# Optimization experiments

Hardware: AMD Instinct MI355X
Metric: run time of the kernel (lower is better)

Reference implementation:

```python
import jax, jax.numpy as jnp
import numpy as np

# ---- static architecture constants (match init_kwargs) ----
B = 64          # batch
N = 64          # n_particles
D = 3           # n_dimensions
H = 256         # hidden_nf
TE = 128        # t_embed_dims
L = 3           # n_layers
SIGMA = 0.5     # data_sigma
MAX_POS = 10000.0
COORDS_RANGE = 15.0  # standard EGNN coords_range; per-layer = COORDS_RANGE/L


def _fc_edges():
    # fully-connected edges (no self loops) within each sample, flattened node ids
    a = np.arange(N)
    r = np.repeat(a, N); c = np.tile(a, N)
    m = r != c
    r0, c0 = r[m], c[m]                      # [N*(N-1)]
    off = (np.arange(B) * N)[:, None]
    rows = (off + r0[None, :]).reshape(-1)   # [B*N*(N-1)]
    cols = (off + c0[None, :]).reshape(-1)
    return jnp.asarray(rows, jnp.int32), jnp.asarray(cols, jnp.int32)


def setup_inputs() -> dict:
    key = jax.random.key(0)
    ks = jax.random.split(key, 20)
    g = lambda k, shape, fan: jax.random.normal(k, shape, jnp.float32) / np.sqrt(fan)
    rows, cols = _fc_edges()
    return {
        'logt': jax.random.normal(ks[0], (B,), jnp.float32),
        'xs':   jax.random.normal(ks[1], (B, N * D), jnp.float32),
        'Wemb': g(ks[2], (TE, H), TE), 'bemb': jnp.zeros((H,), jnp.float32),
        'We1': g(ks[3], (L, 2 * H + 1, H), 2 * H + 1), 'be1': jnp.zeros((L, H), jnp.float32),
        'We2': g(ks[4], (L, H, H), H),                 'be2': jnp.zeros((L, H), jnp.float32),
        'Wa':  g(ks[5], (L, H, 1), H),                 'ba':  jnp.zeros((L, 1), jnp.float32),
        'Wn1': g(ks[6], (L, 2 * H, H), 2 * H),         'bn1': jnp.zeros((L, H), jnp.float32),
        'Wn2': g(ks[7], (L, H, H), H),                 'bn2': jnp.zeros((L, H), jnp.float32),
        'Wc1': g(ks[8], (L, H, H), H),                 'bc1': jnp.zeros((L, H), jnp.float32),
        'Wc2': g(ks[9], (L, H, 1), H) * 1e-3,          # small-init final coord layer
        'rows': rows, 'cols': cols,
    }


def _egnn_net(t_emb, x_flat, Wemb, bemb, We1, be1, We2, be2, Wa, ba,
              Wn1, bn1, Wn2, bn2, Wc1, bc1, Wc2, rows, cols):
    # x_flat: [B*N, D]; t_emb: [B, TE] -> node features [B*N, H]
    num_nodes = B * N
    h = jnp.repeat(t_emb, N, axis=0) @ Wemb + bemb
    x = x_flat
    cr = COORDS_RANGE / L
    for l in range(L):
        diff = x[rows] - x[cols]                              # [E, D]
        radial = jnp.sum(diff * diff, axis=1, keepdims=True)  # [E, 1]
        diff_n = diff / (jnp.sqrt(radial + 1e-8) + 1.0)       # normalized (norm_constant=1)
        eh = jnp.concatenate([h[rows], h[cols], radial], axis=1)
        m = jax.nn.silu(eh @ We1[l] + be1[l])
        m = jax.nn.silu(m @ We2[l] + be2[l])
        m = m * jax.nn.sigmoid(m @ Wa[l] + ba[l])             # attention gate
        # equivariant coordinate update (tanh-bounded)
        s = jax.nn.silu(m @ Wc1[l] + bc1[l])
        trans = diff_n * jnp.tanh(s @ Wc2[l]) * cr            # [E, D]
        x = x + jax.ops.segment_sum(trans, rows, num_segments=num_nodes)
        # node update with residual
        agg = jax.ops.segment_sum(m, rows, num_segments=num_nodes)
        dh = jax.nn.silu(jnp.concatenate([h, agg], axis=1) @ Wn1[l] + bn1[l]) @ Wn2[l] + bn2[l]
        h = h + dh
    vel = (x - x_flat).reshape(B, N, D)
    vel = vel - jnp.mean(vel, axis=1, keepdims=True)          # remove center of gravity
    return vel.reshape(B, N * D)


def reference(logt, xs, Wemb, bemb, We1, be1, We2, be2, Wa, ba,
              Wn1, bn1, Wn2, bn2, Wc1, bc1, Wc2, rows, cols):
    # sinusoidal time embedding of logt/4
    K = TE // 2
    freqs = (1.0 / MAX_POS) ** (jnp.arange(K, dtype=jnp.float32) / K)
    ang = (logt / 4.0)[:, None] * freqs[None, :]
    t_emb = jnp.concatenate([jnp.cos(ang), jnp.sin(ang)], axis=1)  # [B, TE]
    # EDM preconditioning
    t = jnp.exp(logt)[:, None]                                     # [B, 1]
    c_in = 1.0 / jnp.sqrt(SIGMA ** 2 + t ** 2)
    x_flat = (xs * c_in).reshape(B * N, D)
    net_out = _egnn_net(t_emb, x_flat, Wemb, bemb, We1, be1, We2, be2, Wa, ba,
                        Wn1, bn1, Wn2, bn2, Wc1, bc1, Wc2, rows, cols)
    denom = SIGMA ** 2 + t ** 2
    return xs * (SIGMA ** 2) / denom + net_out * (SIGMA * t) / jnp.sqrt(denom)
```

## Files before the change

### kernel.cpp

```cpp
#include <hip/hip_runtime.h>

typedef unsigned short ushort_t;
typedef __attribute__((ext_vector_type(8))) short s8v;
typedef __attribute__((ext_vector_type(4))) float f4v;
typedef __attribute__((ext_vector_type(2))) unsigned int u32x2;
typedef __attribute__((ext_vector_type(4))) unsigned int u32x4;

#define NNODE 4096
#define HID 256
#define CR_L 5.0f
#define ASTR 528
#define ASTR16 (16 * ASTR)
#define NSTR 1056
#define NSTR16 (16 * NSTR)

__device__ __forceinline__ unsigned int cvt2(float lo, float hi) {
  unsigned int r;
  asm("v_cvt_pk_bf16_f32 %0, %1, %2" : "=v"(r) : "v"(lo), "v"(hi));
  return r;
}
__device__ __forceinline__ ushort_t cvt1(float v) {
  unsigned int r;
  asm("v_cvt_pk_bf16_f32 %0, %1, %2" : "=v"(r) : "v"(v), "v"(v));
  return (ushort_t)r;
}
__device__ __forceinline__ float fast_rcp(float x) {
  float r;
  asm("v_rcp_f32 %0, %1" : "=v"(r) : "v"(x));
  return r;
}
__device__ __forceinline__ float silu_f(float v) { return v * fast_rcp(1.0f + __expf(-v)); }
__device__ __forceinline__ float sigm_f(float v) { return fast_rcp(1.0f + __expf(-v)); }

__device__ __forceinline__ void loadB(s8v bd[4], const char* base, int q) {
#pragma unroll
  for (int nt = 0; nt < 4; ++nt)
    bd[nt] = *(const s8v*)(base + nt * 8192 + q * 1024);
}
__device__ __forceinline__ void mfma_step(const char* Ath, int q, const s8v bc[4], f4v acc[4][4]) {
  s8v a[4];
#pragma unroll
  for (int mt = 0; mt < 4; ++mt)
    a[mt] = *(const s8v*)(Ath + mt * ASTR16 + q * 64);
#pragma unroll
  for (int mt = 0; mt < 4; ++mt)
#pragma unroll
    for (int nt = 0; nt < 4; ++nt)
      acc[mt][nt] = __builtin_amdgcn_mfma_f32_16x16x32_bf16(a[mt], bc[nt], acc[mt][nt], 0, 0, 0);
}

__device__ __forceinline__ void gemm64(const char* Ath, const ushort_t* Bth, f4v acc[4][4]) {
#pragma unroll
  for (int ks = 0; ks < 8; ++ks) {
    s8v a[4], bb[4];
#pragma unroll
    for (int mt = 0; mt < 4; ++mt)
      a[mt] = *(const s8v*)(Ath + mt * ASTR16 + ks * 64);
#pragma unroll
    for (int nt = 0; nt < 4; ++nt)
      bb[nt] = *(const s8v*)(Bth + nt * 4096 + ks * 32);
#pragma unroll
    for (int mt = 0; mt < 4; ++mt)
#pragma unroll
      for (int nt = 0; nt < 4; ++nt)
        acc[mt][nt] = __builtin_amdgcn_mfma_f32_16x16x32_bf16(a[mt], bb[nt], acc[mt][nt], 0, 0, 0);
  }
}

__global__ __launch_bounds__(256) void wconv_kernel(
    const float* __restrict__ We1, const float* __restrict__ We2,
    const float* __restrict__ Wc1, const float* __restrict__ Wn1,
    const float* __restrict__ Wn2, ushort_t* __restrict__ wt) {
  int gid = blockIdx.x * 256 + threadIdx.x;
  int l = gid / 458752;
  int r = gid - l * 458752;
  float v;
  if (r < 131072) {
    int part = r >> 16; int rr = r & 65535; int nn = rr >> 8, k = rr & 255;
    v = We1[(l * 513 + part * 256 + k) * 256 + nn];
  } else if (r < 262144) {
    const float* W = (r < 196608) ? We2 : Wc1;
    int rr = (r < 196608) ? (r - 131072) : (r - 196608);
    int ki = rr & 7, ln = (rr >> 3) & 63, f = rr >> 9;
    int ks = f & 7, n16 = f >> 3;
    int al = ln & 15, ag = ln >> 4;
    int nn = n16 * 16 + al, k = ks * 32 + ag * 8 + ki;
    v = W[(l * 256 + k) * 256 + nn];
  } else if (r < 393216) {
    int rr = r - 262144; int nn = rr >> 9, k = rr & 511;
    v = Wn1[(l * 512 + k) * 256 + nn];
  } else {
    int rr = r - 393216; int nn = rr >> 8, k = rr & 255;
    v = Wn2[(l * 256 + k) * 256 + nn];
  }
  wt[gid] = cvt1(v);
}

__global__ __launch_bounds__(256) void embed_kernel(
    const float* __restrict__ logt, const float* __restrict__ xs,
    const float* __restrict__ Wemb, const float* __restrict__ bemb,
    float* __restrict__ h, float* __restrict__ x0) {
  __shared__ float te[128];
  const int b = blockIdx.x, tid = threadIdx.x;
  const float lt = logt[b];
  if (tid < 64) {
    float fr = powf(1e-4f, (float)tid * (1.0f / 64.0f));
    float ang = lt * 0.25f * fr;
    te[tid] = cosf(ang);
    te[tid + 64] = sinf(ang);
  }
  float tt = expf(lt);
  float cin = 1.0f / sqrtf(0.25f + tt * tt);
  if (tid < 192) x0[b * 192 + tid] = xs[b * 192 + tid] * cin;
  __syncthreads();
  float acc = bemb[tid];
  for (int k = 0; k < 128; ++k) acc += te[k] * Wemb[k * 256 + tid];
  float* hp = h + (b * 64) * 256 + tid;
#pragma unroll 4
  for (int nn = 0; nn < 64; ++nn) hp[nn * 256] = acc;
}

__global__ __launch_bounds__(256) void proj_kernel(
    const float* __restrict__ h, const ushort_t* __restrict__ Bt0,
    const ushort_t* __restrict__ Bt1, const float* __restrict__ be1,
    float* __restrict__ p_r, float* __restrict__ p_c) {
  __shared__ u32x4 AbV[64 * ASTR / 16];
  char* Ab = (char*)AbV;
  const int t = threadIdx.x, lane = t & 63, w = t >> 6;
  const int al = lane & 15, ag = lane >> 4;
  const int mat = blockIdx.x & 1;
  const int R0 = (blockIdx.x >> 1) * 64;
  {
    const int j = t & 63, cc = t >> 6;
    const float4* hv = (const float4*)(h + (R0 + j) * 256) + cc * 16;
    u32x4* wb = (u32x4*)(Ab + j * ASTR + cc * 128);
#pragma unroll
    for (int g = 0; g < 8; ++g) {
      float4 v0 = hv[g * 2], v1 = hv[g * 2 + 1];
      u32x4 q;
      q[0] = cvt2(v0.x, v0.y); q[1] = cvt2(v0.z, v0.w);
      q[2] = cvt2(v1.x, v1.y); q[3] = cvt2(v1.z, v1.w);
      wb[g] = q;
    }
  }
  __syncthreads();
  const char* Ath = Ab + al * ASTR + ag * 16;
  const ushort_t* Bth = (mat ? Bt1 : Bt0) + (w * 64 + al) * 256 + ag * 8;
  float* P = mat ? p_c : p_r;
  f4v acc[4][4];
#pragma unroll
  for (int mt = 0; mt < 4; ++mt)
#pragma unroll
    for (int nt = 0; nt < 4; ++nt) acc[mt][nt] = (f4v){0.f, 0.f, 0.f, 0.f};
  gemm64(Ath, Bth, acc);
#pragma unroll
  for (int mt = 0; mt < 4; ++mt)
#pragma unroll
    for (int nt = 0; nt < 4; ++nt) {
      int col = w * 64 + nt * 16 + al;
      float bias = mat ? 0.0f : be1[col];
#pragma unroll
      for (int r = 0; r < 4; ++r) {
        int row = mt * 16 + ag * 4 + r;
        P[(R0 + row) * 256 + col] = acc[mt][nt][r] + bias;
      }
    }
}

__global__ __launch_bounds__(256, 3) void edge_kernel(
    const float* __restrict__ x_in, float* __restrict__ x_out,
    const float* __restrict__ p_r, const float* __restrict__ p_c,
    const float* __restrict__ w_rad,
    const ushort_t* __restrict__ We2t, const float* __restrict__ be2,
    const float* __restrict__ Wa, const float* __restrict__ ba,
    const ushort_t* __restrict__ Wc1t, const float* __restrict__ bc1,
    const float* __restrict__ Wc2, float* __restrict__ agg) {
  __shared__ u32x4 AbV[64 * ASTR / 16];
  char* Ab = (char*)AbV;
  __shared__ float dn[64][3];
  __shared__ float red[4][64];

  const int t = threadIdx.x;
  const int node = ((blockIdx.x & 7) << 9) | (blockIdx.x >> 3);
  const int b = node >> 6, n = node & 63;
  const int lane = t & 63, w = t >> 6;
  const int al = lane & 15, ag = lane >> 4;

  const char* bWe2 = (const char*)We2t + w * 32768 + lane * 16;
  const char* bWc1 = (const char*)Wc1t + w * 32768 + lane * 16;

  s8v b0[4], b1[4], b2[4];
  loadB(b0, bWe2, 0);
  loadB(b1, bWe2, 1);

  float4 pr4 = *(const float4*)(p_r + (node << 8) + 4 * lane);
  float4 wr4 = *(const float4*)(w_rad + 4 * lane);
  float r2_reg;
  {
    const int j = lane;
    const int cl = j < n ? j : j + 1;
    const int nb = (b << 6) + cl;
    const float xi0 = x_in[node * 3], xi1 = x_in[node * 3 + 1], xi2 = x_in[node * 3 + 2];
    const float d0 = xi0 - x_in[nb * 3], d1 = xi1 - x_in[nb * 3 + 1], d2 = xi2 - x_in[nb * 3 + 2];
    r2_reg = d0 * d0 + d1 * d1 + d2 * d2;
    if (w == 0 && j < 63) {
      const float inv = fast_rcp(sqrtf(r2_reg + 1e-8f) + 1.0f);
      dn[j][0] = d0 * inv; dn[j][1] = d1 * inv; dn[j][2] = d2 * inv;
    }
  }

  {
#pragma unroll
    for (int jj = 0; jj < 16; ++jj) {
      const int j = w * 16 + jj;
      u32x2 q2 = {0u, 0u};
      if (j < 63) {
        const int cl = j < n ? j : j + 1;
        const int nb = (b << 6) + cl;
        float4 pc4 = *(const float4*)(p_c + (nb << 8) + 4 * lane);
        const float rj = __shfl(r2_reg, j);
        float v0 = silu_f(pr4.x + pc4.x + rj * wr4.x);
        float v1 = silu_f(pr4.y + pc4.y + rj * wr4.y);
        float v2 = silu_f(pr4.z + pc4.z + rj * wr4.z);
        float v3 = silu_f(pr4.w + pc4.w + rj * wr4.w);
        q2[0] = cvt2(v0, v1); q2[1] = cvt2(v2, v3);
      }
      *(u32x2*)(Ab + j * ASTR + lane * 8) = q2;
    }
  }
  __syncthreads();

  const char* Ath = Ab + al * ASTR + ag * 16;

  f4v acc[4][4];
#pragma unroll
  for (int mt = 0; mt < 4; ++mt)
#pragma unroll
    for (int nt = 0; nt < 4; ++nt) acc[mt][nt] = (f4v){0.f, 0.f, 0.f, 0.f};
  loadB(b2, bWe2, 2); mfma_step(Ath, 0, b0, acc);
  loadB(b0, bWe2, 3); mfma_step(Ath, 1, b1, acc);
  loadB(b1, bWe2, 4); mfma_step(Ath, 2, b2, acc);
  loadB(b2, bWe2, 5); mfma_step(Ath, 3, b0, acc);
  loadB(b0, bWe2, 6); mfma_step(Ath, 4, b1, acc);
  loadB(b1, bWe2, 7); mfma_step(Ath, 5, b2, acc);
  loadB(b2, bWc1, 0); mfma_step(Ath, 6, b0, acc);
  loadB(b0, bWc1, 1); mfma_step(Ath, 7, b1, acc);

  {
    float bb2[4], wa4[4];
#pragma unroll
    for (int nt = 0; nt < 4; ++nt) {
      int col = w * 64 + nt * 16 + al;
      bb2[nt] = be2[col]; wa4[nt] = Wa[col];
    }
    float attp[4][4];
#pragma unroll
    for (int mt = 0; mt < 4; ++mt) {
#pragma unroll
      for (int r = 0; r < 4; ++r) attp[mt][r] = 0.0f;
#pragma unroll
      for (int nt = 0; nt < 4; ++nt) {
#pragma unroll
        for (int r = 0; r < 4; ++r) {
          float v = silu_f(acc[mt][nt][r] + bb2[nt]);
          acc[mt][nt][r] = v;
          attp[mt][r] += v * wa4[nt];
        }
      }
    }
#pragma unroll
    for (int off = 1; off < 16; off <<= 1)
#pragma unroll
      for (int mt = 0; mt < 4; ++mt)
#pragma unroll
        for (int r = 0; r < 4; ++r) attp[mt][r] += __shfl_xor(attp[mt][r], off);
    __syncthreads();
    char* mwb = Ab + (ag * 4) * ASTR + (w * 64 + al) * 2;
#pragma unroll
    for (int mt = 0; mt < 4; ++mt)
#pragma unroll
      for (int nt = 0; nt < 4; ++nt)
#pragma unroll
        for (int r = 0; r < 4; ++r)
          *(ushort_t*)(mwb + mt * ASTR16 + r * ASTR + nt * 32) = cvt1(acc[mt][nt][r]);
    if (al == 0) {
#pragma unroll
      for (int mt = 0; mt < 4; ++mt)
#pragma unroll
        for (int r = 0; r < 4; ++r) red[w][mt * 16 + ag * 4 + r] = attp[mt][r];
    }
  }
  __syncthreads();

  float att_reg;
  {
    float s = red[0][lane] + red[1][lane] + red[2][lane] + red[3][lane] + ba[0];
    att_reg = (lane < 63) ? sigm_f(s) : 0.0f;
  }

  {
    float aggp[4] = {0.f, 0.f, 0.f, 0.f};
#pragma unroll
    for (int mt = 0; mt < 4; ++mt) {
      float a0 = __shfl(att_reg, mt * 16 + ag * 4 + 0);
      float a1 = __shfl(att_reg, mt * 16 + ag * 4 + 1);
      float a2 = __shfl(att_reg, mt * 16 + ag * 4 + 2);
      float a3 = __shfl(att_reg, mt * 16 + ag * 4 + 3);
#pragma unroll
      for (int nt = 0; nt < 4; ++nt)
        aggp[nt] += a0 * acc[mt][nt][0] + a1 * acc[mt][nt][1] +
                    a2 * acc[mt][nt][2] + a3 * acc[mt][nt][3];
    }
#pragma unroll
    for (int nt = 0; nt < 4; ++nt) {
      aggp[nt] += __shfl_xor(aggp[nt], 16);
      aggp[nt] += __shfl_xor(aggp[nt], 32);
    }
    float avv = (ag == 0) ? aggp[0] : (ag == 1) ? aggp[1] : (ag == 2) ? aggp[2] : aggp[3];
    agg[(node << 8) + w * 64 + lane] = avv;
  }

#pragma unroll
  for (int mt = 0; mt < 4; ++mt)
#pragma unroll
    for (int nt = 0; nt < 4; ++nt) acc[mt][nt] = (f4v){0.f, 0.f, 0.f, 0.f};
  loadB(b1, bWc1, 2); mfma_step(Ath, 0, b2, acc);
  loadB(b2, bWc1, 3); mfma_step(Ath, 1, b0, acc);
  loadB(b0, bWc1, 4); mfma_step(Ath, 2, b1, acc);
  loadB(b1, bWc1, 5); mfma_step(Ath, 3, b2, acc);
  loadB(b2, bWc1, 6); mfma_step(Ath, 4, b0, acc);
  loadB(b0, bWc1, 7); mfma_step(Ath, 5, b1, acc);
  mfma_step(Ath, 6, b2, acc);
  mfma_step(Ath, 7, b0, acc);

  {
    float b3[4], wc4[4];
#pragma unroll
    for (int nt = 0; nt < 4; ++nt) {
      int col = w * 64 + nt * 16 + al;
      b3[nt] = bc1[col]; wc4[nt] = Wc2[col];
    }
    float trp[4][4];
#pragma unroll
    for (int mt = 0; mt < 4; ++mt) {
      float a0 = __shfl(att_reg, mt * 16 + ag * 4 + 0);
      float a1 = __shfl(att_reg, mt * 16 + ag * 4 + 1);
      float a2 = __shfl(att_reg, mt * 16 + ag * 4 + 2);
      float a3 = __shfl(att_reg, mt * 16 + ag * 4 + 3);
#pragma unroll
      for (int r = 0; r < 4; ++r) trp[mt][r] = 0.0f;
#pragma unroll
      for (int nt = 0; nt < 4; ++nt) {
        trp[mt][0] += silu_f(a0 * acc[mt][nt][0] + b3[nt]) * wc4[nt];
        trp[mt][1] += silu_f(a1 * acc[mt][nt][1] + b3[nt]) * wc4[nt];
        trp[mt][2] += silu_f(a2 * acc[mt][nt][2] + b3[nt]) * wc4[nt];
        trp[mt][3] += silu_f(a3 * acc[mt][nt][3] + b3[nt]) * wc4[nt];
      }
    }
#pragma unroll
    for (int off = 1; off < 16; off <<= 1)
#pragma unroll
      for (int mt = 0; mt < 4; ++mt)
#pragma unroll
        for (int r = 0; r < 4; ++r) trp[mt][r] += __shfl_xor(trp[mt][r], off);
    if (al == 0) {
#pragma unroll
      for (int mt = 0; mt < 4; ++mt)
#pragma unroll
        for (int r = 0; r < 4; ++r) red[w][mt * 16 + ag * 4 + r] = trp[mt][r];
    }
  }
  __syncthreads();

  if (t < 64) {
    float s = red[0][t] + red[1][t] + red[2][t] + red[3][t];
    float vx = 0.f, vy = 0.f, vz = 0.f;
    if (t < 63) {
      float tj = tanhf(s) * CR_L;
      vx = dn[t][0] * tj; vy = dn[t][1] * tj; vz = dn[t][2] * tj;
    }
#pragma unroll
    for (int off = 1; off < 64; off <<= 1) {
      vx += __shfl_xor(vx, off);
      vy += __shfl_xor(vy, off);
      vz += __shfl_xor(vz, off);
    }
    if (t == 0) {
      x_out[node * 3 + 0] = x_in[node * 3 + 0] + vx;
      x_out[node * 3 + 1] = x_in[node * 3 + 1] + vy;
      x_out[node * 3 + 2] = x_in[node * 3 + 2] + vz;
    }
  }
}

__global__ __launch_bounds__(256) void node_kernel(
    float* __restrict__ h, const float* __restrict__ agg,
    const ushort_t* __restrict__ Wn1t, const float* __restrict__ bn1,
    const ushort_t* __restrict__ Wn2t, const float* __restrict__ bn2) {
  __shared__ u32x4 AbV[64 * NSTR / 16];
  char* Ab = (char*)AbV;
  const int t = threadIdx.x, lane = t & 63, w = t >> 6;
  const int al = lane & 15, ag = lane >> 4;
  const int R0 = blockIdx.x * 64;
  {
    const int j = t & 63, cc = t >> 6;
    u32x4* wb = (u32x4*)(Ab + j * NSTR + cc * 256);
#pragma unroll
    for (int g = 0; g < 16; ++g) {
      int c0 = cc * 128 + g * 8;
      const float* src = (c0 < 256) ? (h + (R0 + j) * 256 + c0)
                                    : (agg + (R0 + j) * 256 + (c0 - 256));
      float4 v0 = *(const float4*)src;
      float4 v1 = *(const float4*)(src + 4);
      u32x4 q;
      q[0] = cvt2(v0.x, v0.y); q[1] = cvt2(v0.z, v0.w);
      q[2] = cvt2(v1.x, v1.y); q[3] = cvt2(v1.z, v1.w);
      wb[g] = q;
    }
  }
  __syncthreads();
  const char* AthN = Ab + al * NSTR + ag * 16;
  const ushort_t* BthA = Wn1t + (w * 64 + al) * 512 + ag * 8;
  f4v acc[4][4];
#pragma unroll
  for (int mt = 0; mt < 4; ++mt)
#pragma unroll
    for (int nt = 0; nt < 4; ++nt) acc[mt][nt] = (f4v){0.f, 0.f, 0.f, 0.f};
#pragma unroll
  for (int ks = 0; ks < 16; ++ks) {
    s8v a[4], bb[4];
#pragma unroll
    for (int mt = 0; mt < 4; ++mt)
      a[mt] = *(const s8v*)(AthN + mt * NSTR16 + ks * 64);
#pragma unroll
    for (int nt = 0; nt < 4; ++nt)
      bb[nt] = *(const s8v*)(BthA + nt * 8192 + ks * 32);
#pragma unroll
    for (int mt = 0; mt < 4; ++mt)
#pragma unroll
      for (int nt = 0; nt < 4; ++nt)
        acc[mt][nt] = __builtin_amdgcn_mfma_f32_16x16x32_bf16(a[mt], bb[nt], acc[mt][nt], 0, 0, 0);
  }
  __syncthreads();
  {
    float bn1c[4];
#pragma unroll
    for (int nt = 0; nt < 4; ++nt) bn1c[nt] = bn1[w * 64 + nt * 16 + al];
    char* mwb = Ab + (ag * 4) * ASTR + (w * 64 + al) * 2;
#pragma unroll
    for (int mt = 0; mt < 4; ++mt)
#pragma unroll
      for (int nt = 0; nt < 4; ++nt)
#pragma unroll
        for (int r = 0; r < 4; ++r) {
          float v = silu_f(acc[mt][nt][r] + bn1c[nt]);
          *(ushort_t*)(mwb + mt * ASTR16 + r * ASTR + nt * 32) = cvt1(v);
        }
  }
  __syncthreads();
  const char* Ath2 = Ab + al * ASTR + ag * 16;
  const ushort_t* BthB = Wn2t + (w * 64 + al) * 256 + ag * 8;
#pragma unroll
  for (int mt = 0; mt < 4; ++mt)
#pragma unroll
    for (int nt = 0; nt < 4; ++nt) acc[mt][nt] = (f4v){0.f, 0.f, 0.f, 0.f};
  gemm64(Ath2, BthB, acc);
  {
    float bn2c[4];
#pragma unroll
    for (int nt = 0; nt < 4; ++nt) bn2c[nt] = bn2[w * 64 + nt * 16 + al];
#pragma unroll
    for (int mt = 0; mt < 4; ++mt)
#pragma unroll
      for (int nt = 0; nt < 4; ++nt) {
        int col = w * 64 + nt * 16 + al;
#pragma unroll
        for (int r = 0; r < 4; ++r) {
          int row = mt * 16 + ag * 4 + r;
          int idx = (R0 + row) * 256 + col;
          h[idx] = h[idx] + acc[mt][nt][r] + bn2c[nt];
        }
      }
  }
}

__global__ __launch_bounds__(64) void final_kernel(
    const float* __restrict__ logt, const float* __restrict__ xs,
    const float* __restrict__ xf, const float* __restrict__ x0,
    float* __restrict__ out) {
  const int b = blockIdx.x, t = threadIdx.x;
  float lt = logt[b], tt = expf(lt);
  float denom = 0.25f + tt * tt;
  float s1 = 0.25f / denom;
  float s2 = 0.5f * tt / sqrtf(denom);
  int node = b * 64 + t;
  float v0 = xf[node * 3 + 0] - x0[node * 3 + 0];
  float v1 = xf[node * 3 + 1] - x0[node * 3 + 1];
  float v2 = xf[node * 3 + 2] - x0[node * 3 + 2];
  float m0 = v0, m1 = v1, m2 = v2;
#pragma unroll
  for (int off = 1; off < 64; off <<= 1) {
    m0 += __shfl_xor(m0, off);
    m1 += __shfl_xor(m1, off);
    m2 += __shfl_xor(m2, off);
  }
  m0 *= (1.0f / 64.0f); m1 *= (1.0f / 64.0f); m2 *= (1.0f / 64.0f);
  out[b * 192 + t * 3 + 0] = xs[b * 192 + t * 3 + 0] * s1 + (v0 - m0) * s2;
  out[b * 192 + t * 3 + 1] = xs[b * 192 + t * 3 + 1] * s1 + (v1 - m1) * s2;
  out[b * 192 + t * 3 + 2] = xs[b * 192 + t * 3 + 2] * s1 + (v2 - m2) * s2;
}

extern "C" void kernel_launch(void* const* d_in, const int* in_sizes, int n_in,
                              void* d_out, int out_size, void* d_ws, size_t ws_size,
                              hipStream_t stream) {
  const float* logt = (const float*)d_in[0];
  const float* xs   = (const float*)d_in[1];
  const float* Wemb = (const float*)d_in[2];
  const float* bemb = (const float*)d_in[3];
  const float* We1  = (const float*)d_in[4];
  const float* be1  = (const float*)d_in[5];
  const float* We2  = (const float*)d_in[6];
  const float* be2  = (const float*)d_in[7];
  const float* Wa   = (const float*)d_in[8];
  const float* ba   = (const float*)d_in[9];
  const float* Wn1  = (const float*)d_in[10];
  const float* bn1  = (const float*)d_in[11];
  const float* Wn2  = (const float*)d_in[12];
  const float* bn2  = (const float*)d_in[13];
  const float* Wc1  = (const float*)d_in[14];
  const float* bc1  = (const float*)d_in[15];
  const float* Wc2  = (const float*)d_in[16];
  float* out = (float*)d_out;

  float* h   = (float*)d_ws;
  float* pr  = h   + NNODE * HID;
  float* pc  = pr  + NNODE * HID;
  float* agg = pc  + NNODE * HID;
  float* x0  = agg + NNODE * HID;
  float* x1  = x0  + 12288;
  float* x2  = x1  + 12288;
  ushort_t* wt = (ushort_t*)(x2 + 12288);

  wconv_kernel<<<5376, 256, 0, stream>>>(We1, We2, Wc1, Wn1, Wn2, wt);
  embed_kernel<<<64, 256, 0, stream>>>(logt, xs, Wemb, bemb, h, x0);

  const float* xin = x0;
  float* xout = x1;
  for (int l = 0; l < 3; ++l) {
    const ushort_t* wl = wt + l * 458752;
    proj_kernel<<<128, 256, 0, stream>>>(h, wl, wl + 65536, be1 + l * 256, pr, pc);
    edge_kernel<<<4096, 256, 0, stream>>>(
        xin, xout, pr, pc,
        We1 + (l * 513 + 512) * 256,
        wl + 131072, be2 + l * 256,
        Wa + l * 256, ba + l,
        wl + 196608, bc1 + l * 256, Wc2 + l * 256, agg);
    node_kernel<<<64, 256, 0, stream>>>(h, agg, wl + 262144, bn1 + l * 256,
                                        wl + 393216, bn2 + l * 256);
    if (l == 0) { xin = x1; xout = x2; }
    else if (l == 1) { xin = x2; xout = x1; }
  }
  final_kernel<<<64, 64, 0, stream>>>(logt, xs, x1, x0, out);
}
```

Before: 472.1 us.

## Pre-swizzle weights for lane-contiguous MFMA loads; halve node tiles; store agg as bf16

The weight conversion now writes the proj, node Wn1 and Wn2 matrices in a lane-packed MFMA fragment layout. It also applies a k-permutation to Wc1 and Wn2 so the activation tiles can be written to shared memory as packed 8-byte bf16 stores instead of scalar 2-byte stores. The proj and node GEMMs use double-buffered B register loads. The node kernel uses 32-row tiles, giving 128 blocks instead of 64. The aggregated messages are stored as bf16, which halves that traffic but adds rounding before the node MLP.

```diff
diff --git a/kernel.cpp b/kernel.cpp
--- a/kernel.cpp
+++ b/kernel.cpp
@@ -37,6 +37,11 @@
   for (int nt = 0; nt < 4; ++nt)
     bd[nt] = *(const s8v*)(base + nt * 8192 + q * 1024);
 }
+__device__ __forceinline__ void loadBn1(s8v bd[4], const char* base, int q) {
+#pragma unroll
+  for (int nt = 0; nt < 4; ++nt)
+    bd[nt] = *(const s8v*)(base + nt * 16384 + q * 1024);
+}
 __device__ __forceinline__ void mfma_step(const char* Ath, int q, const s8v bc[4], f4v acc[4][4]) {
   s8v a[4];
 #pragma unroll
@@ -48,23 +53,27 @@
     for (int nt = 0; nt < 4; ++nt)
       acc[mt][nt] = __builtin_amdgcn_mfma_f32_16x16x32_bf16(a[mt], bc[nt], acc[mt][nt], 0, 0, 0);
 }
-
-__device__ __forceinline__ void gemm64(const char* Ath, const ushort_t* Bth, f4v acc[4][4]) {
-#pragma unroll
-  for (int ks = 0; ks < 8; ++ks) {
-    s8v a[4], bb[4];
-#pragma unroll
-    for (int mt = 0; mt < 4; ++mt)
-      a[mt] = *(const s8v*)(Ath + mt * ASTR16 + ks * 64);
+__device__ __forceinline__ void mfma32_n1(const char* Ath, int q, const s8v bc[4], f4v acc[2][4]) {
+  s8v a[2];
+#pragma unroll
+  for (int mt = 0; mt < 2; ++mt)
+    a[mt] = *(const s8v*)(Ath + mt * NSTR16 + q * 64);
+#pragma unroll
+  for (int mt = 0; mt < 2; ++mt)
 #pragma unroll
     for (int nt = 0; nt < 4; ++nt)
-      bb[nt] = *(const s8v*)(Bth + nt * 4096 + ks * 32);
-#pragma unroll
-    for (int mt = 0; mt < 4; ++mt)
-#pragma unroll
-      for (int nt = 0; nt < 4; ++nt)
-        acc[mt][nt] = __builtin_amdgcn_mfma_f32_16x16x32_bf16(a[mt], bb[nt], acc[mt][nt], 0, 0, 0);
-  }
+      acc[mt][nt] = __builtin_amdgcn_mfma_f32_16x16x32_bf16(a[mt], bc[nt], acc[mt][nt], 0, 0, 0);
+}
+__device__ __forceinline__ void mfma32_a(const char* Ath, int q, const s8v bc[4], f4v acc[2][4]) {
+  s8v a[2];
+#pragma unroll
+  for (int mt = 0; mt < 2; ++mt)
+    a[mt] = *(const s8v*)(Ath + mt * ASTR16 + q * 64);
+#pragma unroll
+  for (int mt = 0; mt < 2; ++mt)
+#pragma unroll
+    for (int nt = 0; nt < 4; ++nt)
+      acc[mt][nt] = __builtin_amdgcn_mfma_f32_16x16x32_bf16(a[mt], bc[nt], acc[mt][nt], 0, 0, 0);
 }
 
 __global__ __launch_bounds__(256) void wconv_kernel(
@@ -75,22 +84,31 @@
   int l = gid / 458752;
   int r = gid - l * 458752;
   float v;
-  if (r < 131072) {
-    int part = r >> 16; int rr = r & 65535; int nn = rr >> 8, k = rr & 255;
-    v = We1[(l * 513 + part * 256 + k) * 256 + nn];
-  } else if (r < 262144) {
-    const float* W = (r < 196608) ? We2 : Wc1;
-    int rr = (r < 196608) ? (r - 131072) : (r - 196608);
+  if (r < 262144) {
+    int m = r >> 16;
+    int rr = r & 65535;
     int ki = rr & 7, ln = (rr >> 3) & 63, f = rr >> 9;
-    int ks = f & 7, n16 = f >> 3;
-    int al = ln & 15, ag = ln >> 4;
+    int ks = f & 7, n16 = f >> 3, al = ln & 15, ag = ln >> 4;
+    int nn = n16 * 16 + al;
+    int kslot = ks * 32 + ag * 8 + ki;
+    int k = (m == 3) ? ((kslot & ~63) | ((kslot & 3) << 4) | ((kslot & 63) >> 2)) : kslot;
+    if (m == 0)      v = We1[(l * 513 + k) * 256 + nn];
+    else if (m == 1) v = We1[(l * 513 + 256 + k) * 256 + nn];
+    else if (m == 2) v = We2[(l * 256 + k) * 256 + nn];
+    else             v = Wc1[(l * 256 + k) * 256 + nn];
+  } else if (r < 393216) {
+    int rr = r - 262144;
+    int ki = rr & 7, ln = (rr >> 3) & 63, f = rr >> 9;
+    int ks = f & 15, n16 = f >> 4, al = ln & 15, ag = ln >> 4;
     int nn = n16 * 16 + al, k = ks * 32 + ag * 8 + ki;
-    v = W[(l * 256 + k) * 256 + nn];
-  } else if (r < 393216) {
-    int rr = r - 262144; int nn = rr >> 9, k = rr & 511;
     v = Wn1[(l * 512 + k) * 256 + nn];
   } else {
-    int rr = r - 393216; int nn = rr >> 8, k = rr & 255;
+    int rr = r - 393216;
+    int ki = rr & 7, ln = (rr >> 3) & 63, f = rr >> 9;
+    int ks = f & 7, n16 = f >> 3, al = ln & 15, ag = ln >> 4;
+    int nn = n16 * 16 + al;
+    int kslot = ks * 32 + ag * 8 + ki;
+    int k = (kslot & ~63) | ((kslot & 3) << 4) | ((kslot & 63) >> 2);
     v = Wn2[(l * 256 + k) * 256 + nn];
   }
   wt[gid] = cvt1(v);
@@ -145,14 +163,23 @@
   }
   __syncthreads();
   const char* Ath = Ab + al * ASTR + ag * 16;
-  const ushort_t* Bth = (mat ? Bt1 : Bt0) + (w * 64 + al) * 256 + ag * 8;
+  const char* Bth = (const char*)(mat ? Bt1 : Bt0) + w * 32768 + lane * 16;
   float* P = mat ? p_c : p_r;
   f4v acc[4][4];
 #pragma unroll
   for (int mt = 0; mt < 4; ++mt)
 #pragma unroll
     for (int nt = 0; nt < 4; ++nt) acc[mt][nt] = (f4v){0.f, 0.f, 0.f, 0.f};
-  gemm64(Ath, Bth, acc);
+  s8v b0[4], b1[4];
+  loadB(b0, Bth, 0); loadB(b1, Bth, 1);
+  mfma_step(Ath, 0, b0, acc); loadB(b0, Bth, 2);
+  mfma_step(Ath, 1, b1, acc); loadB(b1, Bth, 3);
+  mfma_step(Ath, 2, b0, acc); loadB(b0, Bth, 4);
+  mfma_step(Ath, 3, b1, acc); loadB(b1, Bth, 5);
+  mfma_step(Ath, 4, b0, acc); loadB(b0, Bth, 6);
+  mfma_step(Ath, 5, b1, acc); loadB(b1, Bth, 7);
+  mfma_step(Ath, 6, b0, acc);
+  mfma_step(Ath, 7, b1, acc);
 #pragma unroll
   for (int mt = 0; mt < 4; ++mt)
 #pragma unroll
@@ -174,7 +201,7 @@
     const ushort_t* __restrict__ We2t, const float* __restrict__ be2,
     const float* __restrict__ Wa, const float* __restrict__ ba,
     const ushort_t* __restrict__ Wc1t, const float* __restrict__ bc1,
-    const float* __restrict__ Wc2, float* __restrict__ agg) {
+    const float* __restrict__ Wc2, ushort_t* __restrict__ aggb) {
   __shared__ u32x4 AbV[64 * ASTR / 16];
   char* Ab = (char*)AbV;
   __shared__ float dn[64][3];
@@ -275,14 +302,16 @@
 #pragma unroll
         for (int r = 0; r < 4; ++r) attp[mt][r] += __shfl_xor(attp[mt][r], off);
     __syncthreads();
-    char* mwb = Ab + (ag * 4) * ASTR + (w * 64 + al) * 2;
+    char* mwb = Ab + (ag * 4) * ASTR + (w * 64 + al * 4) * 2;
 #pragma unroll
     for (int mt = 0; mt < 4; ++mt)
 #pragma unroll
-      for (int nt = 0; nt < 4; ++nt)
-#pragma unroll
-        for (int r = 0; r < 4; ++r)
-          *(ushort_t*)(mwb + mt * ASTR16 + r * ASTR + nt * 32) = cvt1(acc[mt][nt][r]);
+      for (int r = 0; r < 4; ++r) {
+        u32x2 p;
+        p[0] = cvt2(acc[mt][0][r], acc[mt][1][r]);
+        p[1] = cvt2(acc[mt][2][r], acc[mt][3][r]);
+        *(u32x2*)(mwb + mt * ASTR16 + r * ASTR) = p;
+      }
     if (al == 0) {
 #pragma unroll
       for (int mt = 0; mt < 4; ++mt)
@@ -317,7 +346,7 @@
       aggp[nt] += __shfl_xor(aggp[nt], 32);
     }
     float avv = (ag == 0) ? aggp[0] : (ag == 1) ? aggp[1] : (ag == 2) ? aggp[2] : aggp[3];
-    agg[(node << 8) + w * 64 + lane] = avv;
+    aggb[(node << 8) + w * 64 + lane] = cvt1(avv);
   }
 
 #pragma unroll
@@ -394,83 +423,98 @@
 }
 
 __global__ __launch_bounds__(256) void node_kernel(
-    float* __restrict__ h, const float* __restrict__ agg,
+    float* __restrict__ h, const ushort_t* __restrict__ aggb,
     const ushort_t* __restrict__ Wn1t, const float* __restrict__ bn1,
     const ushort_t* __restrict__ Wn2t, const float* __restrict__ bn2) {
-  __shared__ u32x4 AbV[64 * NSTR / 16];
+  __shared__ u32x4 AbV[32 * NSTR / 16];
   char* Ab = (char*)AbV;
   const int t = threadIdx.x, lane = t & 63, w = t >> 6;
   const int al = lane & 15, ag = lane >> 4;
-  const int R0 = blockIdx.x * 64;
-  {
-    const int j = t & 63, cc = t >> 6;
-    u32x4* wb = (u32x4*)(Ab + j * NSTR + cc * 256);
-#pragma unroll
-    for (int g = 0; g < 16; ++g) {
-      int c0 = cc * 128 + g * 8;
-      const float* src = (c0 < 256) ? (h + (R0 + j) * 256 + c0)
-                                    : (agg + (R0 + j) * 256 + (c0 - 256));
-      float4 v0 = *(const float4*)src;
-      float4 v1 = *(const float4*)(src + 4);
+  const int R0 = blockIdx.x * 32;
+  {
+    const int j = t & 31, cc = t >> 5;
+#pragma unroll
+    for (int g = 0; g < 8; ++g) {
+      int c0 = cc * 64 + g * 8;
       u32x4 q;
-      q[0] = cvt2(v0.x, v0.y); q[1] = cvt2(v0.z, v0.w);
-      q[2] = cvt2(v1.x, v1.y); q[3] = cvt2(v1.z, v1.w);
-      wb[g] = q;
+      if (c0 < 256) {
+        const float4* src = (const float4*)(h + (R0 + j) * 256 + c0);
+        float4 v0 = src[0], v1 = src[1];
+        q[0] = cvt2(v0.x, v0.y); q[1] = cvt2(v0.z, v0.w);
+        q[2] = cvt2(v1.x, v1.y); q[3] = cvt2(v1.z, v1.w);
+      } else {
+        q = *(const u32x4*)(aggb + (R0 + j) * 256 + (c0 - 256));
+      }
+      *(u32x4*)(Ab + j * NSTR + c0 * 2) = q;
     }
   }
   __syncthreads();
   const char* AthN = Ab + al * NSTR + ag * 16;
-  const ushort_t* BthA = Wn1t + (w * 64 + al) * 512 + ag * 8;
-  f4v acc[4][4];
-#pragma unroll
-  for (int mt = 0; mt < 4; ++mt)
+  const char* bW1 = (const char*)Wn1t + w * 65536 + lane * 16;
+  f4v acc[2][4];
+#pragma unroll
+  for (int mt = 0; mt < 2; ++mt)
 #pragma unroll
     for (int nt = 0; nt < 4; ++nt) acc[mt][nt] = (f4v){0.f, 0.f, 0.f, 0.f};
-#pragma unroll
-  for (int ks = 0; ks < 16; ++ks) {
-    s8v a[4], bb[4];
-#pragma unroll
-    for (int mt = 0; mt < 4; ++mt)
-      a[mt] = *(const s8v*)(AthN + mt * NSTR16 + ks * 64);
-#pragma unroll
-    for (int nt = 0; nt < 4; ++nt)
-      bb[nt] = *(const s8v*)(BthA + nt * 8192 + ks * 32);
-#pragma unroll
-    for (int mt = 0; mt < 4; ++mt)
-#pragma unroll
-      for (int nt = 0; nt < 4; ++nt)
-        acc[mt][nt] = __builtin_amdgcn_mfma_f32_16x16x32_bf16(a[mt], bb[nt], acc[mt][nt], 0, 0, 0);
-  }
+  s8v b0[4], b1[4];
+  loadBn1(b0, bW1, 0); loadBn1(b1, bW1, 1);
+  mfma32_n1(AthN, 0, b0, acc);  loadBn1(b0, bW1, 2);
+  mfma32_n1(AthN, 1, b1, acc);  loadBn1(b1, bW1, 3);
+  mfma32_n1(AthN, 2, b0, acc);  loadBn1(b0, bW1, 4);
+  mfma32_n1(AthN, 3, b1, acc);  loadBn1(b1, bW1, 5);
+  mfma32_n1(AthN, 4, b0, acc);  loadBn1(b0, bW1, 6);
+  mfma32_n1(AthN, 5, b1, acc);  loadBn1(b1, bW1, 7);
+  mfma32_n1(AthN, 6, b0, acc);  loadBn1(b0, bW1, 8);
+  mfma32_n1(AthN, 7, b1, acc);  loadBn1(b1, bW1, 9);
+  mfma32_n1(AthN, 8, b0, acc);  loadBn1(b0, bW1, 10);
+  mfma32_n1(AthN, 9, b1, acc);  loadBn1(b1, bW1, 11);
+  mfma32_n1(AthN, 10, b0, acc); loadBn1(b0, bW1, 12);
+  mfma32_n1(AthN, 11, b1, acc); loadBn1(b1, bW1, 13);
+  mfma32_n1(AthN, 12, b0, acc); loadBn1(b0, bW1, 14);
+  mfma32_n1(AthN, 13, b1, acc); loadBn1(b1, bW1, 15);
+  mfma32_n1(AthN, 14, b0, acc);
+  mfma32_n1(AthN, 15, b1, acc);
   __syncthreads();
   {
     float bn1c[4];
 #pragma unroll
     for (int nt = 0; nt < 4; ++nt) bn1c[nt] = bn1[w * 64 + nt * 16 + al];
-    char* mwb = Ab + (ag * 4) * ASTR + (w * 64 + al) * 2;
-#pragma unroll
-    for (int mt = 0; mt < 4; ++mt)
-#pragma unroll
-      for (int nt = 0; nt < 4; ++nt)
-#pragma unroll
-        for (int r = 0; r < 4; ++r) {
-          float v = silu_f(acc[mt][nt][r] + bn1c[nt]);
-          *(ushort_t*)(mwb + mt * ASTR16 + r * ASTR + nt * 32) = cvt1(v);
-        }
+    char* mwb = Ab + (ag * 4) * ASTR + (w * 64 + al * 4) * 2;
+#pragma unroll
+    for (int mt = 0; mt < 2; ++mt)
+#pragma unroll
+      for (int r = 0; r < 4; ++r) {
+        float s0 = silu_f(acc[mt][0][r] + bn1c[0]);
+        float s1 = silu_f(acc[mt][1][r] + bn1c[1]);
+        float s2 = silu_f(acc[mt][2][r] + bn1c[2]);
+        float s3 = silu_f(acc[mt][3][r] + bn1c[3]);
+        u32x2 p; p[0] = cvt2(s0, s1); p[1] = cvt2(s2, s3);
+        *(u32x2*)(mwb + mt * ASTR16 + r * ASTR) = p;
+      }
   }
   __syncthreads();
   const char* Ath2 = Ab + al * ASTR + ag * 16;
-  const ushort_t* BthB = Wn2t + (w * 64 + al) * 256 + ag * 8;
-#pragma unroll
-  for (int mt = 0; mt < 4; ++mt)
-#pragma unroll
-    for (int nt = 0; nt < 4; ++nt) acc[mt][nt] = (f4v){0.f, 0.f, 0.f, 0.f};
-  gemm64(Ath2, BthB, acc);
+  const char* bW2 = (const char*)Wn2t + w * 32768 + lane * 16;
+  f4v acc2[2][4];
+#pragma unroll
+  for (int mt = 0; mt < 2; ++mt)
+#pragma unroll
+    for (int nt = 0; nt < 4; ++nt) acc2[mt][nt] = (f4v){0.f, 0.f, 0.f, 0.f};
+  loadB(b0, bW2, 0); loadB(b1, bW2, 1);
+  mfma32_a(Ath2, 0, b0, acc2); loadB(b0, bW2, 2);
+  mfma32_a(Ath2, 1, b1, acc2); loadB(b1, bW2, 3);
+  mfma32_a(Ath2, 2, b0, acc2); loadB(b0, bW2, 4);
+  mfma32_a(Ath2, 3, b1, acc2); loadB(b1, bW2, 5);
+  mfma32_a(Ath2, 4, b0, acc2); loadB(b0, bW2, 6);
+  mfma32_a(Ath2, 5, b1, acc2); loadB(b1, bW2, 7);
+  mfma32_a(Ath2, 6, b0, acc2);
+  mfma32_a(Ath2, 7, b1, acc2);
   {
     float bn2c[4];
 #pragma unroll
     for (int nt = 0; nt < 4; ++nt) bn2c[nt] = bn2[w * 64 + nt * 16 + al];
 #pragma unroll
-    for (int mt = 0; mt < 4; ++mt)
+    for (int mt = 0; mt < 2; ++mt)
 #pragma unroll
       for (int nt = 0; nt < 4; ++nt) {
         int col = w * 64 + nt * 16 + al;
@@ -478,7 +522,7 @@
         for (int r = 0; r < 4; ++r) {
           int row = mt * 16 + ag * 4 + r;
           int idx = (R0 + row) * 256 + col;
-          h[idx] = h[idx] + acc[mt][nt][r] + bn2c[nt];
+          h[idx] = h[idx] + acc2[mt][nt][r] + bn2c[nt];
         }
       }
   }
@@ -532,13 +576,13 @@
   const float* Wc2  = (const float*)d_in[16];
   float* out = (float*)d_out;
 
-  float* h   = (float*)d_ws;
-  float* pr  = h   + NNODE * HID;
-  float* pc  = pr  + NNODE * HID;
-  float* agg = pc  + NNODE * HID;
-  float* x0  = agg + NNODE * HID;
-  float* x1  = x0  + 12288;
-  float* x2  = x1  + 12288;
+  float* h    = (float*)d_ws;
+  float* pr   = h  + NNODE * HID;
+  float* pc   = pr + NNODE * HID;
+  ushort_t* aggb = (ushort_t*)(pc + NNODE * HID);
+  float* x0   = (float*)(aggb + NNODE * HID);
+  float* x1   = x0 + 12288;
+  float* x2   = x1 + 12288;
   ushort_t* wt = (ushort_t*)(x2 + 12288);
 
   wconv_kernel<<<5376, 256, 0, stream>>>(We1, We2, Wc1, Wn1, Wn2, wt);
@@ -554,9 +598,9 @@
         We1 + (l * 513 + 512) * 256,
         wl + 131072, be2 + l * 256,
         Wa + l * 256, ba + l,
-        wl + 196608, bc1 + l * 256, Wc2 + l * 256, agg);
-    node_kernel<<<64, 256, 0, stream>>>(h, agg, wl + 262144, bn1 + l * 256,
-                                        wl + 393216, bn2 + l * 256);
+        wl + 196608, bc1 + l * 256, Wc2 + l * 256, aggb);
+    node_kernel<<<128, 256, 0, stream>>>(h, aggb, wl + 262144, bn1 + l * 256,
+                                         wl + 393216, bn2 + l * 256);
     if (l == 0) { xin = x1; xout = x2; }
     else if (l == 1) { xin = x2; xout = x1; }
   }
```

Result: faster. 417.8 us (median of 2 runs) (-11.5%).
